# Kernel optimization log

Measured on AMD Instinct MI355X. Metric: run time of the kernel, lower is better.

Reference implementation:

```python
import jax, jax.numpy as jnp
import numpy as np

S = 4096  # source_sequence_size
Q = 4096  # query_sequence_size
E = 2048  # embedding_size
D = 2048  # output_embedding_size


def setup_inputs() -> dict:
    key = jax.random.key(0)
    ks = jax.random.split(key, 9)
    s = 1.0 / np.sqrt(E)
    return {
        "key": jax.random.normal(ks[0], (S, E), jnp.float32),
        "value": jax.random.normal(ks[1], (S, E), jnp.float32),
        "query": jax.random.normal(ks[2], (Q, E), jnp.float32),
        "Wk": jax.random.normal(ks[3], (D, E), jnp.float32) * s,
        "bk": jax.random.normal(ks[4], (D,), jnp.float32) * 0.01,
        "Wq": jax.random.normal(ks[5], (D, E), jnp.float32) * s,
        "bq": jax.random.normal(ks[6], (D,), jnp.float32) * 0.01,
        "Wv": jax.random.normal(ks[7], (D, E), jnp.float32) * s,
        "bv": jax.random.normal(ks[8], (D,), jnp.float32) * 0.01,
    }


def reference(key, value, query, Wk, bk, Wq, bq, Wv, bv):
    # Linear projections (nn.Linear: x @ W.T + b)
    k = key @ Wk.T + bk      # [S, D]
    v = value @ Wv.T + bv    # [S, D]
    q = query @ Wq.T + bq    # [Q, D]
    # Per-query-token attention scores over all source tokens (schema BOTH),
    # then weighted sum over value rows -- vectorized form of the per-token
    # apply_attention_scores loop.
    scale = 1.0 / jnp.sqrt(jnp.asarray(D, q.dtype))
    scores = jax.nn.softmax(jnp.einsum("qd,sd->qs", q, k) * scale, axis=-1)  # [Q, S]
    return jnp.einsum("qs,sd->qd", scores, v)  # [Q, D]
```

## Files before the change

### kernel.cpp

```cpp
#include <hip/hip_runtime.h>

#define S_SEQ 4096
#define Q_SEQ 4096
#define E_DIM 2048
#define D_DIM 2048

typedef __bf16 bf16;
typedef __bf16 bf16x4 __attribute__((ext_vector_type(4)));
typedef __bf16 bf16x8 __attribute__((ext_vector_type(8)));
typedef float f32x4 __attribute__((ext_vector_type(4)));

__global__ __launch_bounds__(256) void cast6(
    const float* __restrict__ i0, const float* __restrict__ i1,
    const float* __restrict__ i2, const float* __restrict__ i3,
    const float* __restrict__ i4, const float* __restrict__ i5,
    bf16* __restrict__ o0, bf16* __restrict__ o1, bf16* __restrict__ o2,
    bf16* __restrict__ o3, bf16* __restrict__ o4, bf16* __restrict__ o5) {
  const float* in;
  bf16* out;
  int n4;
  switch (blockIdx.y) {
    case 0: in = i0; out = o0; n4 = (S_SEQ * E_DIM) / 4; break;
    case 1: in = i1; out = o1; n4 = (S_SEQ * E_DIM) / 4; break;
    case 2: in = i2; out = o2; n4 = (S_SEQ * E_DIM) / 4; break;
    case 3: in = i3; out = o3; n4 = (D_DIM * E_DIM) / 4; break;
    case 4: in = i4; out = o4; n4 = (D_DIM * E_DIM) / 4; break;
    default: in = i5; out = o5; n4 = (D_DIM * E_DIM) / 4; break;
  }
  int i = blockIdx.x * 256 + threadIdx.x;
  if (i < n4) {
    float4 v = reinterpret_cast<const float4*>(in)[i];
    bf16x4 o;
    o[0] = (bf16)v.x; o[1] = (bf16)v.y; o[2] = (bf16)v.z; o[3] = (bf16)v.w;
    *reinterpret_cast<bf16x4*>(out + 4 * (size_t)i) = o;
  }
}

__device__ __forceinline__ void async_copy16(const bf16* g, bf16* l) {
  __builtin_amdgcn_global_load_lds(
      (const __attribute__((address_space(1))) void*)g,
      (__attribute__((address_space(3))) void*)l, 16, 0, 0);
}

__device__ __forceinline__ int swz(int row) {
  return (row & 3) ^ ((row >> 2) & 3);
}

template <bool OUT_BF16>
__device__ __forceinline__ void gemm_body(
    const bf16* __restrict__ A, int lda,
    const bf16* __restrict__ B, int ldb,
    void* __restrict__ C, int ldc,
    const float* __restrict__ bias, int K, int mBase, int nBase) {
  __shared__ __align__(16) bf16 Als[128 * 32];
  __shared__ __align__(16) bf16 Bls[128 * 32];

  const int tid  = threadIdx.x;
  const int wave = tid >> 6;
  const int lane = tid & 63;
  const int quad = lane >> 4;
  const int lrow = lane & 15;
  const int wRow = (wave >> 1) * 64;
  const int wCol = (wave & 1) * 64;

  f32x4 acc[4][4];
#pragma unroll
  for (int i = 0; i < 4; ++i)
#pragma unroll
    for (int j = 0; j < 4; ++j) {
      f32x4 z = {0.f, 0.f, 0.f, 0.f};
      acc[i][j] = z;
    }

  for (int k0 = 0; k0 < K; k0 += 32) {
#pragma unroll
    for (int c = 0; c < 2; ++c) {
      int chunk = c * 256 + tid;
      int row = chunk >> 2;
      int kq = (chunk & 3) ^ swz(row);
      const bf16* g = A + (size_t)(mBase + row) * lda + k0 + kq * 8;
      async_copy16(g, Als + (size_t)(c * 256 + wave * 64) * 8);
    }
#pragma unroll
    for (int c = 0; c < 2; ++c) {
      int chunk = c * 256 + tid;
      int row = chunk >> 2;
      int kq = (chunk & 3) ^ swz(row);
      const bf16* g = B + (size_t)(nBase + row) * ldb + k0 + kq * 8;
      async_copy16(g, Bls + (size_t)(c * 256 + wave * 64) * 8);
    }
    __syncthreads();

    bf16x8 af[4], bfr[4];
#pragma unroll
    for (int i = 0; i < 4; ++i) {
      int r = wRow + i * 16 + lrow;
      af[i] = *(const bf16x8*)(Als + (size_t)r * 32 + (quad ^ swz(r)) * 8);
    }
#pragma unroll
    for (int j = 0; j < 4; ++j) {
      int r = wCol + j * 16 + lrow;
      bfr[j] = *(const bf16x8*)(Bls + (size_t)r * 32 + (quad ^ swz(r)) * 8);
    }
#pragma unroll
    for (int i = 0; i < 4; ++i)
#pragma unroll
      for (int j = 0; j < 4; ++j)
        acc[i][j] = __builtin_amdgcn_mfma_f32_16x16x32_bf16(af[i], bfr[j], acc[i][j], 0, 0, 0);
    __syncthreads();
  }

#pragma unroll
  for (int j = 0; j < 4; ++j) {
    const int cn = nBase + wCol + j * 16 + lrow;
    float bj = 0.f;
    if (OUT_BF16) bj = bias[cn];
#pragma unroll
    for (int i = 0; i < 4; ++i) {
      const int rbase = mBase + wRow + i * 16 + quad * 4;
#pragma unroll
      for (int r = 0; r < 4; ++r) {
        if (OUT_BF16)
          ((bf16*)C)[(size_t)(rbase + r) * ldc + cn] = (bf16)(acc[i][j][r] + bj);
        else
          ((float*)C)[(size_t)(rbase + r) * ldc + cn] = acc[i][j][r];
      }
    }
  }
}

__global__ __launch_bounds__(256, 2) void gemm_bt_f32(
    const bf16* __restrict__ A, int lda,
    const bf16* __restrict__ B, int ldb,
    float* __restrict__ C, int ldc, int K) {
  gemm_body<false>(A, lda, B, ldb, (void*)C, ldc, nullptr, K,
                   blockIdx.y * 128, blockIdx.x * 128);
}

__global__ __launch_bounds__(256, 2) void proj_gemm(
    const bf16* __restrict__ xk, const bf16* __restrict__ xq,
    const bf16* __restrict__ xv,
    const bf16* __restrict__ Wk, const bf16* __restrict__ Wq,
    const bf16* __restrict__ Wv,
    const float* __restrict__ bk, const float* __restrict__ bq,
    const float* __restrict__ bv,
    bf16* __restrict__ ok, bf16* __restrict__ oq, bf16* __restrict__ ov) {
  const bf16 *A, *W;
  const float* b;
  bf16* o;
  switch (blockIdx.z) {
    case 0: A = xk; W = Wk; b = bk; o = ok; break;
    case 1: A = xq; W = Wq; b = bq; o = oq; break;
    default: A = xv; W = Wv; b = bv; o = ov; break;
  }
  gemm_body<true>(A, E_DIM, W, E_DIM, (void*)o, D_DIM, b, E_DIM,
                  blockIdx.y * 128, blockIdx.x * 128);
}

__global__ __launch_bounds__(256) void transpose_bf16(
    const bf16* __restrict__ in, bf16* __restrict__ out) {
  __shared__ bf16 tile[64][66];
  const int t = threadIdx.x;
  const int c0 = blockIdx.x * 64;
  const int r0 = blockIdx.y * 64;
  const int col = t & 63;
  const int r4 = t >> 6;
#pragma unroll
  for (int i = 0; i < 16; ++i) {
    int rr = i * 4 + r4;
    tile[rr][col] = in[(size_t)(r0 + rr) * D_DIM + c0 + col];
  }
  __syncthreads();
#pragma unroll
  for (int i = 0; i < 16; ++i) {
    int rr = i * 4 + r4;
    out[(size_t)(c0 + rr) * S_SEQ + r0 + col] = tile[col][rr];
  }
}

__global__ __launch_bounds__(256) void softmax_rows(
    const float* __restrict__ logits, bf16* __restrict__ P, float scale) {
  __shared__ float red[8];
  const int r = blockIdx.x;
  const int t = threadIdx.x;
  const int wid = t >> 6;
  const int lane = t & 63;
  const float4* src4 = (const float4*)(logits + (size_t)r * S_SEQ);

  float4 v[4];
  float lmax = -3.4e38f;
#pragma unroll
  for (int i = 0; i < 4; ++i) {
    v[i] = src4[t + i * 256];
    lmax = fmaxf(fmaxf(fmaxf(lmax, v[i].x), fmaxf(v[i].y, v[i].z)), v[i].w);
  }
#pragma unroll
  for (int off = 32; off > 0; off >>= 1)
    lmax = fmaxf(lmax, __shfl_down(lmax, off, 64));
  if (lane == 0) red[wid] = lmax;
  __syncthreads();
  if (t == 0) red[4] = fmaxf(fmaxf(red[0], red[1]), fmaxf(red[2], red[3]));
  __syncthreads();
  const float rmax = red[4];

  float lsum = 0.f;
#pragma unroll
  for (int i = 0; i < 4; ++i) {
    v[i].x = __expf((v[i].x - rmax) * scale);
    v[i].y = __expf((v[i].y - rmax) * scale);
    v[i].z = __expf((v[i].z - rmax) * scale);
    v[i].w = __expf((v[i].w - rmax) * scale);
    lsum += v[i].x + v[i].y + v[i].z + v[i].w;
  }
#pragma unroll
  for (int off = 32; off > 0; off >>= 1)
    lsum += __shfl_down(lsum, off, 64);
  if (lane == 0) red[wid] = lsum;
  __syncthreads();
  if (t == 0) red[5] = red[0] + red[1] + red[2] + red[3];
  __syncthreads();
  const float inv = 1.0f / red[5];

  bf16x4* dst4 = (bf16x4*)(P + (size_t)r * (2 * S_SEQ));
#pragma unroll
  for (int i = 0; i < 4; ++i) {
    bf16x4 o;
    o[0] = (bf16)(v[i].x * inv);
    o[1] = (bf16)(v[i].y * inv);
    o[2] = (bf16)(v[i].z * inv);
    o[3] = (bf16)(v[i].w * inv);
    dst4[t + i * 256] = o;
  }
}

extern "C" void kernel_launch(void* const* d_in, const int* in_sizes, int n_in,
                              void* d_out, int out_size, void* d_ws, size_t ws_size,
                              hipStream_t stream) {
  const float* key   = (const float*)d_in[0];
  const float* value = (const float*)d_in[1];
  const float* query = (const float*)d_in[2];
  const float* Wk = (const float*)d_in[3];
  const float* bk = (const float*)d_in[4];
  const float* Wq = (const float*)d_in[5];
  const float* bq = (const float*)d_in[6];
  const float* Wv = (const float*)d_in[7];
  const float* bv = (const float*)d_in[8];

  const size_t MB = 1ull << 20;
  char* ws = (char*)d_ws;
  bf16* key_bf   = (bf16*)(ws + 0 * MB);
  bf16* value_bf = (bf16*)(ws + 16 * MB);
  bf16* query_bf = (bf16*)(ws + 32 * MB);
  bf16* Wk_bf    = (bf16*)(ws + 48 * MB);
  bf16* Wq_bf    = (bf16*)(ws + 56 * MB);
  bf16* Wv_bf    = (bf16*)(ws + 64 * MB);
  bf16* k_bf     = (bf16*)(ws + 72 * MB);
  bf16* q_bf     = (bf16*)(ws + 88 * MB);
  bf16* v_bf     = (bf16*)(ws + 104 * MB);
  bf16* vT_bf    = (bf16*)(ws + 120 * MB);
  float* logits  = (float*)(ws + 0 * MB);
  bf16* P        = (bf16*)(ws + 0 * MB);

  dim3 blk(256);

  cast6<<<dim3(8192, 6), blk, 0, stream>>>(
      key, value, query, Wk, Wq, Wv,
      key_bf, value_bf, query_bf, Wk_bf, Wq_bf, Wv_bf);

  proj_gemm<<<dim3(D_DIM / 128, S_SEQ / 128, 3), blk, 0, stream>>>(
      key_bf, query_bf, value_bf, Wk_bf, Wq_bf, Wv_bf, bk, bq, bv,
      k_bf, q_bf, v_bf);

  transpose_bf16<<<dim3(D_DIM / 64, S_SEQ / 64), blk, 0, stream>>>(v_bf, vT_bf);

  gemm_bt_f32<<<dim3(S_SEQ / 128, Q_SEQ / 128), blk, 0, stream>>>(
      q_bf, D_DIM, k_bf, D_DIM, logits, S_SEQ, D_DIM);

  const float scale = 0.022097086912079608f;
  softmax_rows<<<Q_SEQ, blk, 0, stream>>>(logits, P, scale);

  gemm_bt_f32<<<dim3(D_DIM / 128, Q_SEQ / 128), blk, 0, stream>>>(
      P, 2 * S_SEQ, vT_bf, S_SEQ, (float*)d_out, D_DIM, S_SEQ);
}
```

Measured before the change: 491.5 us.

## Enlarge GEMM tiles to 256x128, remap blocks per XCD, drop LDS swizzle

The GEMM tile grows from 128x128 to 256x128, so each wave computes 128x64 outputs with 8x4 MFMA accumulators. This raises arithmetic intensity per LDS load and halves the number of blocks. Launches become 1D, and a remap groups tiles sharing A rows and B columns onto the same XCD to improve L2 reuse. The XOR swizzle on LDS rows is removed, which simplifies addressing but risks LDS bank conflicts on the fragment reads. Register pressure also rises with launch bounds still (256,2), so spilling is possible.

```diff
diff --git a/kernel.cpp b/kernel.cpp
--- a/kernel.cpp
+++ b/kernel.cpp
@@ -42,8 +42,11 @@
       (__attribute__((address_space(3))) void*)l, 16, 0, 0);
 }
 
-__device__ __forceinline__ int swz(int row) {
-  return (row & 3) ^ ((row >> 2) & 3);
+__device__ __forceinline__ void xcd_remap(int id, int nt, int& m, int& n) {
+  int xcd = id & 7;
+  int lid = id >> 3;
+  m = (xcd & 1) * 8 + (lid & 7);
+  n = (xcd >> 1) * (nt >> 2) + (lid >> 3);
 }
 
 template <bool OUT_BF16>
@@ -52,7 +55,7 @@
     const bf16* __restrict__ B, int ldb,
     void* __restrict__ C, int ldc,
     const float* __restrict__ bias, int K, int mBase, int nBase) {
-  __shared__ __align__(16) bf16 Als[128 * 32];
+  __shared__ __align__(16) bf16 Als[256 * 32];
   __shared__ __align__(16) bf16 Bls[128 * 32];
 
   const int tid  = threadIdx.x;
@@ -60,12 +63,12 @@
   const int lane = tid & 63;
   const int quad = lane >> 4;
   const int lrow = lane & 15;
-  const int wRow = (wave >> 1) * 64;
+  const int wRow = (wave >> 1) * 128;
   const int wCol = (wave & 1) * 64;
 
-  f32x4 acc[4][4];
-#pragma unroll
-  for (int i = 0; i < 4; ++i)
+  f32x4 acc[8][4];
+#pragma unroll
+  for (int i = 0; i < 8; ++i)
 #pragma unroll
     for (int j = 0; j < 4; ++j) {
       f32x4 z = {0.f, 0.f, 0.f, 0.f};
@@ -74,36 +77,28 @@
 
   for (int k0 = 0; k0 < K; k0 += 32) {
 #pragma unroll
+    for (int c = 0; c < 4; ++c) {
+      int chunk = c * 256 + tid;
+      const bf16* g = A + (size_t)(mBase + (chunk >> 2)) * lda + k0 + (chunk & 3) * 8;
+      async_copy16(g, Als + (size_t)(c * 256 + wave * 64) * 8);
+    }
+#pragma unroll
     for (int c = 0; c < 2; ++c) {
       int chunk = c * 256 + tid;
-      int row = chunk >> 2;
-      int kq = (chunk & 3) ^ swz(row);
-      const bf16* g = A + (size_t)(mBase + row) * lda + k0 + kq * 8;
-      async_copy16(g, Als + (size_t)(c * 256 + wave * 64) * 8);
-    }
-#pragma unroll
-    for (int c = 0; c < 2; ++c) {
-      int chunk = c * 256 + tid;
-      int row = chunk >> 2;
-      int kq = (chunk & 3) ^ swz(row);
-      const bf16* g = B + (size_t)(nBase + row) * ldb + k0 + kq * 8;
+      const bf16* g = B + (size_t)(nBase + (chunk >> 2)) * ldb + k0 + (chunk & 3) * 8;
       async_copy16(g, Bls + (size_t)(c * 256 + wave * 64) * 8);
     }
     __syncthreads();
 
-    bf16x8 af[4], bfr[4];
-#pragma unroll
-    for (int i = 0; i < 4; ++i) {
-      int r = wRow + i * 16 + lrow;
-      af[i] = *(const bf16x8*)(Als + (size_t)r * 32 + (quad ^ swz(r)) * 8);
-    }
-#pragma unroll
-    for (int j = 0; j < 4; ++j) {
-      int r = wCol + j * 16 + lrow;
-      bfr[j] = *(const bf16x8*)(Bls + (size_t)r * 32 + (quad ^ swz(r)) * 8);
-    }
-#pragma unroll
-    for (int i = 0; i < 4; ++i)
+    bf16x8 af[8], bfr[4];
+#pragma unroll
+    for (int i = 0; i < 8; ++i)
+      af[i] = *(const bf16x8*)(Als + (size_t)(wRow + i * 16 + lrow) * 32 + quad * 8);
+#pragma unroll
+    for (int j = 0; j < 4; ++j)
+      bfr[j] = *(const bf16x8*)(Bls + (size_t)(wCol + j * 16 + lrow) * 32 + quad * 8);
+#pragma unroll
+    for (int i = 0; i < 8; ++i)
 #pragma unroll
       for (int j = 0; j < 4; ++j)
         acc[i][j] = __builtin_amdgcn_mfma_f32_16x16x32_bf16(af[i], bfr[j], acc[i][j], 0, 0, 0);
@@ -116,7 +111,7 @@
     float bj = 0.f;
     if (OUT_BF16) bj = bias[cn];
 #pragma unroll
-    for (int i = 0; i < 4; ++i) {
+    for (int i = 0; i < 8; ++i) {
       const int rbase = mBase + wRow + i * 16 + quad * 4;
 #pragma unroll
       for (int r = 0; r < 4; ++r) {
@@ -132,9 +127,10 @@
 __global__ __launch_bounds__(256, 2) void gemm_bt_f32(
     const bf16* __restrict__ A, int lda,
     const bf16* __restrict__ B, int ldb,
-    float* __restrict__ C, int ldc, int K) {
-  gemm_body<false>(A, lda, B, ldb, (void*)C, ldc, nullptr, K,
-                   blockIdx.y * 128, blockIdx.x * 128);
+    float* __restrict__ C, int ldc, int K, int nt) {
+  int m, n;
+  xcd_remap(blockIdx.x, nt, m, n);
+  gemm_body<false>(A, lda, B, ldb, (void*)C, ldc, nullptr, K, m * 256, n * 128);
 }
 
 __global__ __launch_bounds__(256, 2) void proj_gemm(
@@ -153,8 +149,10 @@
     case 1: A = xq; W = Wq; b = bq; o = oq; break;
     default: A = xv; W = Wv; b = bv; o = ov; break;
   }
+  int m, n;
+  xcd_remap(blockIdx.x, 16, m, n);
   gemm_body<true>(A, E_DIM, W, E_DIM, (void*)o, D_DIM, b, E_DIM,
-                  blockIdx.y * 128, blockIdx.x * 128);
+                  m * 256, n * 128);
 }
 
 __global__ __launch_bounds__(256) void transpose_bf16(
@@ -267,18 +265,18 @@
       key, value, query, Wk, Wq, Wv,
       key_bf, value_bf, query_bf, Wk_bf, Wq_bf, Wv_bf);
 
-  proj_gemm<<<dim3(D_DIM / 128, S_SEQ / 128, 3), blk, 0, stream>>>(
+  proj_gemm<<<dim3(256, 1, 3), blk, 0, stream>>>(
       key_bf, query_bf, value_bf, Wk_bf, Wq_bf, Wv_bf, bk, bq, bv,
       k_bf, q_bf, v_bf);
 
   transpose_bf16<<<dim3(D_DIM / 64, S_SEQ / 64), blk, 0, stream>>>(v_bf, vT_bf);
 
-  gemm_bt_f32<<<dim3(S_SEQ / 128, Q_SEQ / 128), blk, 0, stream>>>(
-      q_bf, D_DIM, k_bf, D_DIM, logits, S_SEQ, D_DIM);
+  gemm_bt_f32<<<dim3(512), blk, 0, stream>>>(
+      q_bf, D_DIM, k_bf, D_DIM, logits, S_SEQ, D_DIM, 32);
 
   const float scale = 0.022097086912079608f;
   softmax_rows<<<Q_SEQ, blk, 0, stream>>>(logits, P, scale);
 
-  gemm_bt_f32<<<dim3(D_DIM / 128, Q_SEQ / 128), blk, 0, stream>>>(
-      P, 2 * S_SEQ, vT_bf, S_SEQ, (float*)d_out, D_DIM, S_SEQ);
-}
+  gemm_bt_f32<<<dim3(256), blk, 0, stream>>>(
+      P, 2 * S_SEQ, vT_bf, S_SEQ, (float*)d_out, D_DIM, S_SEQ, 16);
+}
```

After: 555.5 us. +13.0%, slower.
